# Kernel tuning notes

Measured on AMD Instinct MI355X. Metric: run time of the kernel, lower is better.

## Reference

```python
import jax, jax.numpy as jnp
import numpy as np

GAMMA = 0.5          # cfg.distribution_loss.triplet_loss_gamma
POS_RADIUS = 0.6     # cfg.fine_loss.positive_radius
BIG = 1e12

B, K = 4096, 64      # node correspondences, knn points per node
N = K + 1            # matching_scores has one slack row/col


def setup_inputs() -> dict:
    key = jax.random.key(0)
    k1, k2, k3, k4, k5 = jax.random.split(key, 5)
    pos_pts = jax.random.normal(k1, (B, K, 3), dtype=jnp.float32)
    # anchor points near positives so some pairs fall inside positive_radius
    anc_pts = pos_pts + 0.3 * jax.random.normal(k2, (B, K, 3), dtype=jnp.float32)
    pos_masks = jax.random.uniform(k3, (B, K)) < 0.9
    anc_masks = jax.random.uniform(k4, (B, K)) < 0.9
    matching_scores = jax.random.normal(k5, (B, N, N), dtype=jnp.float32)
    transform = jnp.eye(4, dtype=jnp.float32)  # rigid SE(3); identity keeps pos/neg masks realistic
    return {
        'pos_node_corr_knn_points': pos_pts,
        'anc_node_corr_knn_points': anc_pts,
        'pos_node_corr_knn_masks': pos_masks,
        'anc_node_corr_knn_masks': anc_masks,
        'matching_scores': matching_scores,
        'transform': transform,
    }


def _apply_transform(points, transform):
    R = transform[:3, :3]
    t = transform[:3, 3]
    return jnp.einsum('bkd,ed->bke', points, R) + t


def _pairwise_sq_dist(x, y):
    # (b,n,3),(b,m,3) -> (b,n,m) squared distances
    x2 = jnp.sum(x * x, axis=-1)
    y2 = jnp.sum(y * y, axis=-1)
    xy = jnp.einsum('bnd,bmd->bnm', x, y)
    return x2[:, :, None] - 2.0 * xy + y2[:, None, :]


def reference(pos_node_corr_knn_points, anc_node_corr_knn_points,
              pos_node_corr_knn_masks, anc_node_corr_knn_masks,
              matching_scores, transform):
    b, n, m = matching_scores.shape
    anc = _apply_transform(anc_node_corr_knn_points, transform)
    dists = _pairwise_sq_dist(pos_node_corr_knn_points, anc)  # (b, n-1, m-1)

    gt_masks = pos_node_corr_knn_masks[:, :, None] & anc_node_corr_knn_masks[:, None, :]
    gt_corr = (dists < POS_RADIUS ** 2) & gt_masks
    gt_neg = dists > (2.0 * POS_RADIUS) ** 2
    row_none = jnp.sum(gt_corr, axis=2) == 0   # (b, n-1): rows w/o correspondence -> slack col
    col_none = jnp.sum(gt_corr, axis=1) == 0   # (b, m-1): cols w/o correspondence -> slack row

    pos_mask = (jnp.zeros((b, n, m), dtype=bool)
                .at[:, :-1, :-1].set(gt_corr)
                .at[:, :-1, -1].set(row_none)
                .at[:, -1, :-1].set(col_none))
    neg_mask = (jnp.zeros((b, n, m), dtype=bool)
                .at[:, :-1, :-1].set(gt_neg)
                .at[:, :-1, -1].set(~row_none)
                .at[:, -1, :-1].set(~col_none))

    ms = matching_scores

    # ---- row direction (over pos knn rows, all m cols) ----
    pm = pos_mask[:, :-1, :]
    nm = neg_mask[:, :-1, :]
    ms_r = ms[:, :-1, :]
    pos_score = jnp.sum(jnp.where(pm, -ms_r, 0.0), axis=2) / jnp.sum(pm, axis=2)  # (b, n-1); count>=1
    neg_score = jnp.where(nm, -ms_r, BIG)                                          # (b, n-1, m)
    gap1 = pos_score[:, :, None] - neg_score
    per1 = jnp.log(jnp.sum(jnp.maximum(gap1 + GAMMA, 0.0), axis=2) + 1.0)          # (b, n-1)
    keep1 = pos_score != BIG
    loss1 = jnp.sum(jnp.where(keep1, per1, 0.0)) / jnp.maximum(jnp.sum(keep1), 1)

    # ---- column direction (over anc knn cols, all n rows) ----
    pmc = pos_mask[:, :, :-1]
    nmc = neg_mask[:, :, :-1]
    ms_c = ms[:, :, :-1]
    pos_score_inv = jnp.sum(jnp.where(pmc, -ms_c, 0.0), axis=1) / jnp.sum(pmc, axis=1)  # (b, m-1)
    neg_score_inv = jnp.where(nmc, -ms_c, BIG)                                           # (b, n, m-1)
    gap2 = jnp.transpose(pos_score_inv[:, None, :] - neg_score_inv, (0, 2, 1))           # (b, m-1, n)
    per2 = jnp.log(jnp.sum(jnp.maximum(gap2 + GAMMA, 0.0), axis=2) + 1.0)                # (b, m-1)
    keep2 = pos_score_inv != BIG
    loss2 = jnp.sum(jnp.where(keep2, per2, 0.0)) / jnp.maximum(jnp.sum(keep2), 1)

    return (loss1 + loss2) / 2.0
```

## Files before the change

kernel.cpp:

```cpp
#include <hip/hip_runtime.h>


#define R2_POS 0.36f
#define R2_NEG 1.44f
#define GAMMA_C 0.5f
#define NBATCH 4096
#define NBLOCKS (NBATCH / 2)
#define NPART (NBLOCKS * 4)

__device__ __forceinline__ int maskbit(const void* p, int i, int mode) {
    if (mode == 0) return ((const unsigned*)p)[i] != 0u;
    if (mode == 1) return ((const unsigned short*)p)[i] != 0;
    return ((const unsigned char*)p)[i] != 0;
}

__global__ __launch_bounds__(256)
void fused_kernel(const float* __restrict__ posp,
                  const float* __restrict__ ancp,
                  const void* __restrict__ pmp,
                  const void* __restrict__ amp,
                  const float* __restrict__ msp,
                  const float* __restrict__ xfp,
                  float* __restrict__ partials) {
    __shared__ float tiles[8450];
    __shared__ float4 ancs[128];
    __shared__ float4 poss[128];

    const int tid = threadIdx.x;
    const int blk = blockIdx.x;
    const int w = tid >> 6;
    const int l = tid & 63;
    const int lb = w >> 1;
    const int role = w & 1;
    const int b = blk * 2 + lb;

    unsigned mw0 = ((const unsigned*)pmp)[l];
    bool okw = (mw0 == 0u) || (mw0 == 1u) || (mw0 == 0x3F800000u);
    unsigned hh0 = mw0 & 0xFFFFu, hh1 = mw0 >> 16;
    bool okh = (hh0 == 0u || hh0 == 0x3F80u) && (hh1 == 0u || hh1 == 0x3F80u);
    int mmode = (__ballot(okw) == ~0ULL) ? 0 : ((__ballot(okh) == ~0ULL) ? 1 : 2);

    float T[12];
#pragma unroll
    for (int e = 0; e < 3; ++e)
#pragma unroll
        for (int d = 0; d < 4; ++d) T[e * 4 + d] = xfp[e * 4 + d];

    const int pb = (b * 64 + l) * 3;
    const float px = posp[pb], py = posp[pb + 1], pz = posp[pb + 2];
    const float r0 = ancp[pb], r1 = ancp[pb + 1], r2 = ancp[pb + 2];
    const float ax = T[0] * r0 + T[1] * r1 + T[2]  * r2 + T[3];
    const float ay = T[4] * r0 + T[5] * r1 + T[6]  * r2 + T[7];
    const float az = T[8] * r0 + T[9] * r1 + T[10] * r2 + T[11];

    const int mi = b * 64 + l;
    const unsigned long long pmM = __ballot(maskbit(pmp, mi, mmode) != 0);
    const unsigned long long amM = __ballot(maskbit(amp, mi, mmode) != 0);

    if (role == 0) ancs[lb * 64 + l] = make_float4(ax, ay, az, 0.f);
    else           poss[lb * 64 + l] = make_float4(px, py, pz, 0.f);

    {
        const float2* src = (const float2*)(msp + (size_t)blk * 8450);
        float2* dst = (float2*)tiles;
#pragma unroll
        for (int k = 0; k < 17; ++k) {
            int idx = tid + 256 * k;
            if (idx < 4225) dst[idx] = src[idx];
        }
    }
    __syncthreads();

    const float* tile = tiles + lb * 4225;
    float result;

    if (role == 0) {
        const float* row = tile + l * 65;
        const float4* anc4 = ancs + lb * 64;
        const bool pmL = (pmM >> l) & 1ULL;
        float psum = 0.f; int pcnt = 0;
        unsigned long long negm = 0ULL;
#pragma unroll 16
        for (int j = 0; j < 64; ++j) {
            float v = row[j];
            float4 a = anc4[j];
            float dx = px - a.x, dy = py - a.y, dz = pz - a.z;
            float d2 = dx * dx + dy * dy + dz * dz;
            bool pos = pmL && ((amM >> j) & 1ULL) && (d2 < R2_POS);
            if (pos) { psum -= v; pcnt++; }
            if (d2 > R2_NEG) negm |= (1ULL << j);
        }
        const float slack = row[64];
        const float ps = pcnt ? psum / (float)pcnt : -slack;
        float hv = 0.f;
#pragma unroll 16
        for (int j = 0; j < 64; ++j)
            if ((negm >> j) & 1ULL) hv += fmaxf(ps + row[j] + GAMMA_C, 0.f);
        if (pcnt) hv += fmaxf(ps + slack + GAMMA_C, 0.f);
        result = __logf(hv + 1.f);
    } else {
        const float4* pos4 = poss + lb * 64;
        const bool amL = (amM >> l) & 1ULL;
        float psum = 0.f; int pcnt = 0;
        unsigned long long negm = 0ULL;
#pragma unroll 16
        for (int r = 0; r < 64; ++r) {
            float v = tile[r * 65 + l];
            float4 p = pos4[r];
            float dx = p.x - ax, dy = p.y - ay, dz = p.z - az;
            float d2 = dx * dx + dy * dy + dz * dz;
            bool pos = ((pmM >> r) & 1ULL) && amL && (d2 < R2_POS);
            if (pos) { psum -= v; pcnt++; }
            if (d2 > R2_NEG) negm |= (1ULL << r);
        }
        const float slack = tile[64 * 65 + l];
        const float ps = pcnt ? psum / (float)pcnt : -slack;
        float hv = 0.f;
#pragma unroll 16
        for (int r = 0; r < 64; ++r)
            if ((negm >> r) & 1ULL)
                hv += fmaxf(ps + tile[r * 65 + l] + GAMMA_C, 0.f);
        if (pcnt) hv += fmaxf(ps + slack + GAMMA_C, 0.f);
        result = __logf(hv + 1.f);
    }

#pragma unroll
    for (int off = 1; off < 64; off <<= 1)
        result += __shfl_xor(result, off, 64);
    if (l == 0) partials[blk * 4 + w] = result;
}

__global__ void finalize_kernel(const float* __restrict__ partials,
                                unsigned* __restrict__ out) {
    __shared__ float red[4];
    const int tid = threadIdx.x;
    float s = 0.f;
    for (int i = tid; i < NPART; i += 256) s += partials[i];
#pragma unroll
    for (int off = 1; off < 64; off <<= 1) s += __shfl_xor(s, off, 64);
    if ((tid & 63) == 0) red[tid >> 6] = s;
    __syncthreads();
    if (tid == 0) {
        float tot = red[0] + red[1] + red[2] + red[3];
        float loss = tot * (1.0f / (2.0f * NBATCH * 64.0f));
        unsigned bits = __float_as_uint(loss);
        unsigned h = (bits + 0x7FFFu + ((bits >> 16) & 1u)) >> 16;
        out[0] = (h << 16) | h;
    }
}

extern "C" void kernel_launch(void* const* d_in, const int* in_sizes, int n_in,
                              void* d_out, int out_size, void* d_ws, size_t ws_size,
                              hipStream_t stream) {
    (void)in_sizes; (void)n_in; (void)out_size; (void)ws_size;
    const float* posp = (const float*)d_in[0];
    const float* ancp = (const float*)d_in[1];
    const void* pmp = d_in[2];
    const void* amp = d_in[3];
    const float* msp = (const float*)d_in[4];
    const float* xfp = (const float*)d_in[5];

    fused_kernel<<<NBLOCKS, 256, 0, stream>>>(posp, ancp, pmp, amp, msp, xfp,
                                              (float*)d_ws);
    finalize_kernel<<<1, 256, 0, stream>>>((const float*)d_ws,
                                           (unsigned*)d_out);
}
```

Before: 146.6 us.

## Use one block per batch with fp16 shared-memory score tile

Each block now handles one batch item with 128 threads instead of two items with 256 threads, so the grid doubles. The matching-score tile is converted to half2 as it is stored in shared memory, halving LDS use so more blocks can be resident per CU. The 64-bit negative mask is split into two 32-bit words to reduce register pressure. Rounding scores to fp16 changes numerics slightly; the output is rounded to bf16, which may absorb the error.

```diff
diff --git a/kernel.cpp b/kernel.cpp
--- a/kernel.cpp
+++ b/kernel.cpp
@@ -1,12 +1,12 @@
 #include <hip/hip_runtime.h>
+#include <hip/hip_fp16.h>
 
 
 #define R2_POS 0.36f
 #define R2_NEG 1.44f
 #define GAMMA_C 0.5f
 #define NBATCH 4096
-#define NBLOCKS (NBATCH / 2)
-#define NPART (NBLOCKS * 4)
+#define NPART (NBATCH * 2)
 
 __device__ __forceinline__ int maskbit(const void* p, int i, int mode) {
     if (mode == 0) return ((const unsigned*)p)[i] != 0u;
@@ -14,7 +14,7 @@
     return ((const unsigned char*)p)[i] != 0;
 }
 
-__global__ __launch_bounds__(256)
+__global__ __launch_bounds__(128, 8)
 void fused_kernel(const float* __restrict__ posp,
                   const float* __restrict__ ancp,
                   const void* __restrict__ pmp,
@@ -22,17 +22,15 @@
                   const float* __restrict__ msp,
                   const float* __restrict__ xfp,
                   float* __restrict__ partials) {
-    __shared__ float tiles[8450];
-    __shared__ float4 ancs[128];
-    __shared__ float4 poss[128];
+    __shared__ __half2 tile2[2114];
+    __shared__ float4 ancs[64];
+    __shared__ float4 poss[64];
 
     const int tid = threadIdx.x;
-    const int blk = blockIdx.x;
+    const int b = blockIdx.x;
     const int w = tid >> 6;
     const int l = tid & 63;
-    const int lb = w >> 1;
-    const int role = w & 1;
-    const int b = blk * 2 + lb;
+    const int ofs = b & 1;
 
     unsigned mw0 = ((const unsigned*)pmp)[l];
     bool okw = (mw0 == 0u) || (mw0 == 1u) || (mw0 == 0x3F800000u);
@@ -57,69 +55,75 @@
     const unsigned long long pmM = __ballot(maskbit(pmp, mi, mmode) != 0);
     const unsigned long long amM = __ballot(maskbit(amp, mi, mmode) != 0);
 
-    if (role == 0) ancs[lb * 64 + l] = make_float4(ax, ay, az, 0.f);
-    else           poss[lb * 64 + l] = make_float4(px, py, pz, 0.f);
+    if (w == 0) ancs[l] = make_float4(ax, ay, az, 0.f);
+    else        poss[l] = make_float4(px, py, pz, 0.f);
 
     {
-        const float2* src = (const float2*)(msp + (size_t)blk * 8450);
-        float2* dst = (float2*)tiles;
+        const float2* src = (const float2*)(msp + (size_t)b * 4225 - ofs);
 #pragma unroll
         for (int k = 0; k < 17; ++k) {
-            int idx = tid + 256 * k;
-            if (idx < 4225) dst[idx] = src[idx];
+            int idx = tid + 128 * k;
+            if (idx < 2113) tile2[idx] = __float22half2_rn(src[idx]);
         }
     }
     __syncthreads();
 
-    const float* tile = tiles + lb * 4225;
+    const __half* t = ((const __half*)tile2) + ofs;
     float result;
 
-    if (role == 0) {
-        const float* row = tile + l * 65;
-        const float4* anc4 = ancs + lb * 64;
+    if (w == 0) {
+        const __half* row = t + l * 65;
         const bool pmL = (pmM >> l) & 1ULL;
         float psum = 0.f; int pcnt = 0;
-        unsigned long long negm = 0ULL;
+        unsigned nlo = 0u, nhi = 0u;
 #pragma unroll 16
         for (int j = 0; j < 64; ++j) {
-            float v = row[j];
-            float4 a = anc4[j];
+            float v = __half2float(row[j]);
+            float4 a = ancs[j];
             float dx = px - a.x, dy = py - a.y, dz = pz - a.z;
             float d2 = dx * dx + dy * dy + dz * dz;
             bool pos = pmL && ((amM >> j) & 1ULL) && (d2 < R2_POS);
             if (pos) { psum -= v; pcnt++; }
-            if (d2 > R2_NEG) negm |= (1ULL << j);
+            bool neg = d2 > R2_NEG;
+            if (j < 32) nlo |= (neg ? (1u << j) : 0u);
+            else        nhi |= (neg ? (1u << (j - 32)) : 0u);
         }
-        const float slack = row[64];
+        const float slack = __half2float(row[64]);
         const float ps = pcnt ? psum / (float)pcnt : -slack;
         float hv = 0.f;
 #pragma unroll 16
-        for (int j = 0; j < 64; ++j)
-            if ((negm >> j) & 1ULL) hv += fmaxf(ps + row[j] + GAMMA_C, 0.f);
+        for (int j = 0; j < 32; ++j)
+            if ((nlo >> j) & 1u) hv += fmaxf(ps + __half2float(row[j]) + GAMMA_C, 0.f);
+#pragma unroll 16
+        for (int j = 32; j < 64; ++j)
+            if ((nhi >> (j - 32)) & 1u) hv += fmaxf(ps + __half2float(row[j]) + GAMMA_C, 0.f);
         if (pcnt) hv += fmaxf(ps + slack + GAMMA_C, 0.f);
         result = __logf(hv + 1.f);
     } else {
-        const float4* pos4 = poss + lb * 64;
         const bool amL = (amM >> l) & 1ULL;
         float psum = 0.f; int pcnt = 0;
-        unsigned long long negm = 0ULL;
+        unsigned nlo = 0u, nhi = 0u;
 #pragma unroll 16
         for (int r = 0; r < 64; ++r) {
-            float v = tile[r * 65 + l];
-            float4 p = pos4[r];
+            float v = __half2float(t[r * 65 + l]);
+            float4 p = poss[r];
             float dx = p.x - ax, dy = p.y - ay, dz = p.z - az;
             float d2 = dx * dx + dy * dy + dz * dz;
             bool pos = ((pmM >> r) & 1ULL) && amL && (d2 < R2_POS);
             if (pos) { psum -= v; pcnt++; }
-            if (d2 > R2_NEG) negm |= (1ULL << r);
+            bool neg = d2 > R2_NEG;
+            if (r < 32) nlo |= (neg ? (1u << r) : 0u);
+            else        nhi |= (neg ? (1u << (r - 32)) : 0u);
         }
-        const float slack = tile[64 * 65 + l];
+        const float slack = __half2float(t[64 * 65 + l]);
         const float ps = pcnt ? psum / (float)pcnt : -slack;
         float hv = 0.f;
 #pragma unroll 16
-        for (int r = 0; r < 64; ++r)
-            if ((negm >> r) & 1ULL)
-                hv += fmaxf(ps + tile[r * 65 + l] + GAMMA_C, 0.f);
+        for (int r = 0; r < 32; ++r)
+            if ((nlo >> r) & 1u) hv += fmaxf(ps + __half2float(t[r * 65 + l]) + GAMMA_C, 0.f);
+#pragma unroll 16
+        for (int r = 32; r < 64; ++r)
+            if ((nhi >> (r - 32)) & 1u) hv += fmaxf(ps + __half2float(t[r * 65 + l]) + GAMMA_C, 0.f);
         if (pcnt) hv += fmaxf(ps + slack + GAMMA_C, 0.f);
         result = __logf(hv + 1.f);
     }
@@ -127,7 +131,8 @@
 #pragma unroll
     for (int off = 1; off < 64; off <<= 1)
         result += __shfl_xor(result, off, 64);
-    if (l == 0) partials[blk * 4 + w] = result;
+    if (l == 0) partials[b * 2 + w] = result;
+
 }
 
 __global__ void finalize_kernel(const float* __restrict__ partials,
@@ -160,8 +165,8 @@
     const float* msp = (const float*)d_in[4];
     const float* xfp = (const float*)d_in[5];
 
-    fused_kernel<<<NBLOCKS, 256, 0, stream>>>(posp, ancp, pmp, amp, msp, xfp,
-                                              (float*)d_ws);
+    fused_kernel<<<NBATCH, 128, 0, stream>>>(posp, ancp, pmp, amp, msp, xfp,
+                                             (float*)d_ws);
     finalize_kernel<<<1, 256, 0, stream>>>((const float*)d_ws,
                                            (unsigned*)d_out);
 }
```

New measurement: 148.8 us. About the same (+1.5%).
